# Performance work log

Hardware: AMD Instinct MI355X
Metric: run time of the kernel (lower is better)

Reference implementation:

```python
import jax, jax.numpy as jnp
import numpy as np
from jax.ops import segment_sum

N = 100000   # total nodes
M = 50000    # propagated subset size (len(index))
E = 600000   # edges over the subset graph
D = 128      # embedding_size
EPS = 1e-8
N_LAYERS = 3  # self.LayerNums


def setup_inputs() -> dict:
    key = jax.random.key(0)
    ks = jax.random.split(key, 12)
    features = jax.random.normal(ks[0], (N, D), dtype=jnp.float32)
    index = jnp.arange(M, dtype=jnp.int64)  # subset of nodes that get propagated
    edge_row = jax.random.randint(ks[1], (E,), 0, M, dtype=jnp.int64)
    edge_col = jax.random.randint(ks[2], (E,), 0, M, dtype=jnp.int64)
    edge_val = jax.random.uniform(ks[3], (E,), dtype=jnp.float32)
    # MLP prediction weights: D -> D//2 -> D//4 -> D//6 -> 1 (last no bias)
    def xavier(k, fan_in, fan_out):
        lim = jnp.sqrt(6.0 / (fan_in + fan_out)).astype(jnp.float32)
        return jax.random.uniform(k, (fan_in, fan_out), jnp.float32, -lim, lim)
    W1 = xavier(ks[4], D, D // 2); b1 = jnp.zeros((D // 2,), jnp.float32)
    W2 = xavier(ks[5], D // 2, D // 4); b2 = jnp.zeros((D // 4,), jnp.float32)
    W3 = xavier(ks[6], D // 4, D // 6); b3 = jnp.zeros((D // 6,), jnp.float32)
    W4 = xavier(ks[7], D // 6, 1)
    return {"features": features, "index": index, "edge_row": edge_row,
            "edge_col": edge_col, "edge_val": edge_val,
            "W1": W1, "b1": b1, "W2": W2, "b2": b2, "W3": W3, "b3": b3, "W4": W4}


def _gcn_layer(features, index, row, col, val):
    # symmetric normalization: d = rowsum(A)+eps; A' = d^-1/2 A d^-1/2
    deg = segment_sum(val, row, num_segments=M)
    d_inv_sqrt = jax.lax.rsqrt(deg + EPS)
    nval = val * d_inv_sqrt[row] * d_inv_sqrt[col]
    sub = features[index]                      # [M, D] subset_features
    msg = sub[col] * nval[:, None]             # [E, D]
    out = segment_sum(msg, row, num_segments=M)  # spmm -> [M, D]
    # new_features[index] = out; untouched rows keep original features
    return features.at[index].set(out)


def reference(features, index, edge_row, edge_col, edge_val,
              W1, b1, W2, b2, W3, b3, W4):
    x = features
    for _ in range(N_LAYERS):
        x = _gcn_layer(x, index, edge_row, edge_col, edge_val)
    # MLP prediction head (eval mode: dropout off), LeakyReLU slope 0.01
    h = jax.nn.leaky_relu(x @ W1 + b1, 0.01)
    h = jax.nn.leaky_relu(h @ W2 + b2, 0.01)
    h = jax.nn.leaky_relu(h @ W3 + b3, 0.01)
    return jax.nn.sigmoid(h @ W4)              # [N, 1]
```

## Files before the change

kernel.cpp:

```cpp
#include <hip/hip_runtime.h>
#include <math.h>

#define NN 100000
#define MM 50000
#define EE 600000
#define DD 128
#define NB 196
#define NNP 100096
#define EE4 750000

typedef short bf16x8 __attribute__((ext_vector_type(8)));
typedef float f32x4 __attribute__((ext_vector_type(4)));

__device__ __forceinline__ float bl(unsigned u) { return __uint_as_float(u << 16); }
__device__ __forceinline__ float bh(unsigned u) { return __uint_as_float(u & 0xFFFF0000u); }
__device__ __forceinline__ unsigned rne(float f) {
    unsigned u = __float_as_uint(f);
    return (u + 0x7FFFu + ((u >> 16) & 1u)) >> 16;
}
__device__ __forceinline__ unsigned pk2(float a, float b) { return rne(a) | (rne(b) << 16); }

__device__ __forceinline__ void fmab8(float v, uint4 u, float* a) {
    a[0] = fmaf(v, bl(u.x), a[0]); a[1] = fmaf(v, bh(u.x), a[1]);
    a[2] = fmaf(v, bl(u.y), a[2]); a[3] = fmaf(v, bh(u.y), a[3]);
    a[4] = fmaf(v, bl(u.z), a[4]); a[5] = fmaf(v, bh(u.z), a[5]);
    a[6] = fmaf(v, bl(u.w), a[6]); a[7] = fmaf(v, bh(u.w), a[7]);
}

__device__ __forceinline__ void fma21(float h, const float* wrow, float* a) {
    #pragma unroll
    for (int j = 0; j < 21; ++j) a[j] = fmaf(h, wrow[j], a[j]);
}

__global__ void deg_count_kernel(const int* __restrict__ row, const float* __restrict__ val,
                                 unsigned long long* __restrict__ dcpack,
                                 int* __restrict__ slot, int* __restrict__ invidx) {
    int e = blockIdx.x * 256 + threadIdx.x;
    if (e < NN) invidx[e] = -1;
    if (e < EE) {
        int r = row[e];
        unsigned long long add = (1ULL << 44) | (unsigned long long)(val[e] * 4294967296.0f);
        unsigned long long old = atomicAdd(&dcpack[r], add);
        slot[e] = (int)(old >> 44);
    }
}

__global__ void fused_setup_kernel(const unsigned long long* __restrict__ dcpack,
                                   float* __restrict__ dis,
                                   const int* __restrict__ index, int* __restrict__ invidx,
                                   int* __restrict__ cnt, int* __restrict__ blockhist) {
    __shared__ int lh[256];
    int tid = threadIdx.x;
    int i = blockIdx.x * 256 + tid;
    lh[tid] = 0;
    __syncthreads();
    if (i < MM) {
        unsigned long long pkv = dcpack[i];
        int v = (int)(pkv >> 44);
        float dsum = (float)(pkv & ((1ULL << 44) - 1)) * (1.0f / 4294967296.0f);
        dis[i] = rsqrtf(dsum + 1e-8f);
        invidx[index[i]] = i;
        cnt[i] = v;
        atomicAdd(&lh[min(v, 255)], 1);
    }
    __syncthreads();
    blockhist[tid * NB + blockIdx.x] = lh[tid];
}

__global__ void scan_bins_kernel(const int* __restrict__ blockhist,
                                 int* __restrict__ blockoff, int* __restrict__ total) {
    int d = blockIdx.x;
    int lane = threadIdx.x;
    int carry = 0;
    for (int base = 0; base < NB; base += 64) {
        int b = base + lane;
        int v = (b < NB) ? blockhist[d * NB + b] : 0;
        int x = v;
        #pragma unroll
        for (int off = 1; off < 64; off <<= 1) {
            int t = __shfl_up(x, off, 64);
            if (lane >= off) x += t;
        }
        if (b < NB) blockoff[d * NB + b] = carry + x - v;
        carry += __shfl(x, 63);
    }
    if (lane == 0) total[d] = carry;
}

__global__ void sort_rows_kernel(const int* __restrict__ cnt, const int* __restrict__ blockoff,
                                 const int* __restrict__ total, const int* __restrict__ index,
                                 int4* __restrict__ meta, int* __restrict__ row_s4) {
    __shared__ int lh[256], sbin[256], spad[256], ws[8];
    int tid = threadIdx.x, lane = tid & 63, w = tid >> 6;
    lh[tid] = 0;
    int t = total[tid];
    int v1 = t, v2 = t * ((tid + 3) & ~3);
    int x1 = v1, x2 = v2;
    #pragma unroll
    for (int off = 1; off < 64; off <<= 1) {
        int t1 = __shfl_up(x1, off, 64);
        int t2 = __shfl_up(x2, off, 64);
        if (lane >= off) { x1 += t1; x2 += t2; }
    }
    if (lane == 63) { ws[w] = x1; ws[4 + w] = x2; }
    __syncthreads();
    int a1 = 0, a2 = 0;
    for (int q = 0; q < w; ++q) { a1 += ws[q]; a2 += ws[4 + q]; }
    sbin[tid] = a1 + x1 - v1;
    spad[tid] = a2 + x2 - v2;
    __syncthreads();
    int i = blockIdx.x * 256 + tid;
    if (i < MM) {
        int d = cnt[i], c = min(d, 255);
        int lrank = atomicAdd(&lh[c], 1);
        int k = blockoff[c * NB + blockIdx.x] + lrank;
        int spos = sbin[c] + k;
        int s4 = spad[c] + k * ((d + 3) & ~3);
        meta[MM - 1 - spos] = make_int4(s4, d, i, index[i]);
        row_s4[i] = s4;
    }
}

__global__ void scatter_kernel(const int* __restrict__ row, const int* __restrict__ col,
                               const float* __restrict__ val, const float* __restrict__ dis,
                               const int* __restrict__ row_s4, const int* __restrict__ slot,
                               int* __restrict__ col_s, float* __restrict__ val_s) {
    int e = blockIdx.x * 256 + threadIdx.x;
    if (e < EE) {
        int r = row[e], c = col[e];
        int pos = row_s4[r] + slot[e];
        col_s[pos] = c;
        val_s[pos] = val[e] * dis[r] * dis[c];
    }
}

__global__ void cvt_kernel(const float* __restrict__ feat, const int* __restrict__ index,
                           const int* __restrict__ invidx,
                           unsigned* __restrict__ X0b, unsigned* __restrict__ Xfull,
                           const float* __restrict__ W1, const float* __restrict__ W2,
                           unsigned* __restrict__ W1b, unsigned* __restrict__ W2b) {
    int i = blockIdx.x * 256 + threadIdx.x;
    int n = i >> 6, u = i & 63;
    if (n < NN && invidx[n] < 0) {
        float2 f = ((const float2*)feat)[(size_t)n * 64 + u];
        Xfull[(size_t)n * 64 + u] = pk2(f.x, f.y);
    }
    if (i < MM * 64) {
        int idx = index[n];
        float2 f = ((const float2*)feat)[(size_t)idx * 64 + u];
        X0b[i] = pk2(f.x, f.y);
    }
    if (i < 4096) {
        int j = i >> 6, kp = i & 63;
        W1b[i] = pk2(W1[(2 * kp) * 64 + j], W1[(2 * kp + 1) * 64 + j]);
    } else if (i < 5120) {
        int t = i - 4096;
        int j = t >> 5, kp = t & 31;
        W2b[t] = pk2(W2[(2 * kp) * 32 + j], W2[(2 * kp + 1) * 32 + j]);
    }
}

__global__ __launch_bounds__(256) void spmm_kernel(
    const int4* __restrict__ meta, const int* __restrict__ cols,
    const float* __restrict__ vals, const unsigned short* __restrict__ X,
    unsigned short* __restrict__ Y, int use_remap) {
    int lane = threadIdx.x & 63;
    int wid = threadIdx.x >> 6;
    int g = lane >> 4, sub = lane & 15;
    int ri = blockIdx.x * 16 + wid * 4 + g;
    bool valid = (ri < MM);
    int rc = valid ? ri : (MM - 1);
    int4 mt = meta[rc];
    int s = mt.x, d = mt.y;
    const uint4* __restrict__ X4 = (const uint4*)X;
    float a[8] = {0.f, 0.f, 0.f, 0.f, 0.f, 0.f, 0.f, 0.f};
    int e4 = s + d;
    for (int base = s; base < e4; base += 4) {
        int4 c4 = *(const int4*)(cols + base);
        float4 v4 = *(const float4*)(vals + base);
        uint4 u0 = X4[c4.x * 16 + sub];
        uint4 u1 = X4[c4.y * 16 + sub];
        uint4 u2 = X4[c4.z * 16 + sub];
        uint4 u3 = X4[c4.w * 16 + sub];
        fmab8(v4.x, u0, a);
        fmab8(v4.y, u1, a);
        fmab8(v4.z, u2, a);
        fmab8(v4.w, u3, a);
    }
    if (valid) {
        int dst = use_remap ? mt.w : mt.z;
        uint4 o;
        o.x = pk2(a[0], a[1]); o.y = pk2(a[2], a[3]);
        o.z = pk2(a[4], a[5]); o.w = pk2(a[6], a[7]);
        ((uint4*)Y)[dst * 16 + sub] = o;
    }
}

__global__ __launch_bounds__(256) void mlp_kernel(
    const unsigned* __restrict__ Xfull,
    const unsigned* __restrict__ W1b, const float* __restrict__ b1,
    const unsigned* __restrict__ W2b, const float* __restrict__ b2,
    const float* __restrict__ W3, const float* __restrict__ b3,
    const float* __restrict__ W4, float* __restrict__ out) {
    __shared__ float hls[4 * 1088];
    int tid = threadIdx.x;
    int lane = tid & 63, w = tid >> 6;
    int p = lane & 15, q = lane >> 4;
    float* hw = hls + w * 1088;
    int nb = blockIdx.x * 64;
    int node = nb + w * 16 + p;

    bf16x8 af[4];
    #pragma unroll
    for (int kc = 0; kc < 4; ++kc) {
        uint4 u = *(const uint4*)(Xfull + (size_t)node * 64 + kc * 16 + q * 4);
        af[kc] = *(const bf16x8*)&u;
    }
    f32x4 acc[4];
    #pragma unroll
    for (int jt = 0; jt < 4; ++jt) {
        float bv = b1[jt * 16 + p];
        acc[jt][0] = bv; acc[jt][1] = bv; acc[jt][2] = bv; acc[jt][3] = bv;
    }
    #pragma unroll
    for (int jt = 0; jt < 4; ++jt) {
        #pragma unroll
        for (int kc = 0; kc < 4; ++kc) {
            uint4 u = *(const uint4*)(W1b + (jt * 16 + p) * 64 + kc * 16 + q * 4);
            bf16x8 bf = *(const bf16x8*)&u;
            acc[jt] = __builtin_amdgcn_mfma_f32_16x16x32_bf16(af[kc], bf, acc[jt], 0, 0, 0);
        }
    }
    #pragma unroll
    for (int jt = 0; jt < 4; ++jt) {
        #pragma unroll
        for (int r = 0; r < 4; ++r) {
            float v = acc[jt][r];
            v = v > 0.f ? v : 0.01f * v;
            hw[(q * 4 + r) * 68 + jt * 16 + p] = v;
        }
    }
    bf16x8 a2f[2];
    #pragma unroll
    for (int kc = 0; kc < 2; ++kc) {
        const float* hp = hw + p * 68 + kc * 32 + q * 8;
        f32x4 v0 = *(const f32x4*)hp;
        f32x4 v1 = *(const f32x4*)(hp + 4);
        uint4 uu = make_uint4(pk2(v0[0], v0[1]), pk2(v0[2], v0[3]),
                              pk2(v1[0], v1[1]), pk2(v1[2], v1[3]));
        a2f[kc] = *(const bf16x8*)&uu;
    }
    f32x4 acc2[2];
    #pragma unroll
    for (int jt = 0; jt < 2; ++jt) {
        float bv = b2[jt * 16 + p];
        acc2[jt][0] = bv; acc2[jt][1] = bv; acc2[jt][2] = bv; acc2[jt][3] = bv;
        #pragma unroll
        for (int kc = 0; kc < 2; ++kc) {
            uint4 u = *(const uint4*)(W2b + (jt * 16 + p) * 32 + kc * 16 + q * 4);
            bf16x8 bf = *(const bf16x8*)&u;
            acc2[jt] = __builtin_amdgcn_mfma_f32_16x16x32_bf16(a2f[kc], bf, acc2[jt], 0, 0, 0);
        }
    }
    #pragma unroll
    for (int jt = 0; jt < 2; ++jt) {
        #pragma unroll
        for (int r = 0; r < 4; ++r) {
            float v = acc2[jt][r];
            v = v > 0.f ? v : 0.01f * v;
            hw[(q * 4 + r) * 36 + jt * 16 + p] = v;
        }
    }
    float a3[21];
    #pragma unroll
    for (int j = 0; j < 21; ++j) a3[j] = b3[j];
    #pragma unroll 4
    for (int k = 0; k < 32; ++k) {
        float hk = hw[p * 36 + k];
        fma21(hk, W3 + k * 21, a3);
    }
    float s = 0.f;
    #pragma unroll
    for (int j = 0; j < 21; ++j) {
        float vj = a3[j] > 0.f ? a3[j] : 0.01f * a3[j];
        s = fmaf(vj, W4[j], s);
    }
    if (q == 0) {
        int n = nb + w * 16 + p;
        if (n < NN) out[n] = 1.f / (1.f + expf(-s));
    }
}

extern "C" void kernel_launch(void* const* d_in, const int* in_sizes, int n_in,
                              void* d_out, int out_size, void* d_ws, size_t ws_size,
                              hipStream_t stream) {
    const float* feat = (const float*)d_in[0];
    const int*   index = (const int*)d_in[1];
    const int*   erow = (const int*)d_in[2];
    const int*   ecol = (const int*)d_in[3];
    const float* evalp = (const float*)d_in[4];
    const float* W1 = (const float*)d_in[5];
    const float* b1 = (const float*)d_in[6];
    const float* W2 = (const float*)d_in[7];
    const float* b2 = (const float*)d_in[8];
    const float* W3 = (const float*)d_in[9];
    const float* b3 = (const float*)d_in[10];
    const float* W4 = (const float*)d_in[11];
    float* out = (float*)d_out;

    char* ws = (char*)d_ws;
    size_t off = 0;
    auto alloc = [&](size_t bytes) -> void* {
        void* p = ws + off;
        off += (bytes + 255) & ~(size_t)255;
        return p;
    };
    unsigned long long* dcpack = (unsigned long long*)alloc((size_t)MM * 8);
    int*   col_s   = (int*)  alloc((size_t)EE4 * 4);
    float* val_s   = (float*)alloc((size_t)EE4 * 4);
    size_t zero_span = (size_t)((char*)val_s - (char*)dcpack) + (size_t)EE4 * 4;

    float* dis     = (float*)alloc((size_t)MM * 4);
    int*   cnt     = (int*)  alloc((size_t)MM * 4);
    int*   slot    = (int*)  alloc((size_t)EE * 4);
    int*   invidx  = (int*)  alloc((size_t)NN * 4);
    int*   row_s4  = (int*)  alloc((size_t)MM * 4);
    int*   blockhist = (int*)alloc((size_t)256 * NB * 4);
    int*   blockoff  = (int*)alloc((size_t)256 * NB * 4);
    int*   total     = (int*)alloc((size_t)256 * 4);
    int4*  meta      = (int4*)alloc((size_t)MM * 16);
    unsigned* W1b  = (unsigned*)alloc(4096 * 4);
    unsigned* W2b  = (unsigned*)alloc(1024 * 4);
    unsigned*       X0b   = (unsigned*)      alloc((size_t)MM * DD * 2);
    unsigned short* Xa    = (unsigned short*)alloc((size_t)MM * DD * 2);
    unsigned short* Xb    = (unsigned short*)alloc((size_t)MM * DD * 2);
    unsigned*       Xfull = (unsigned*)      alloc((size_t)NNP * DD * 2);

    hipMemsetAsync(dcpack, 0, zero_span, stream);

    deg_count_kernel<<<(EE + 255) / 256, 256, 0, stream>>>(erow, evalp, dcpack, slot, invidx);
    fused_setup_kernel<<<NB, 256, 0, stream>>>(dcpack, dis, index, invidx, cnt, blockhist);
    scan_bins_kernel<<<256, 64, 0, stream>>>(blockhist, blockoff, total);
    sort_rows_kernel<<<NB, 256, 0, stream>>>(cnt, blockoff, total, index, meta, row_s4);
    scatter_kernel<<<(EE + 255) / 256, 256, 0, stream>>>(erow, ecol, evalp, dis,
                                                         row_s4, slot, col_s, val_s);
    cvt_kernel<<<(NN * 64 + 255) / 256, 256, 0, stream>>>(feat, index, invidx, X0b, Xfull,
                                                          W1, W2, W1b, W2b);

    spmm_kernel<<<(MM + 15) / 16, 256, 0, stream>>>(meta, col_s, val_s,
                                                    (const unsigned short*)X0b, Xa, 0);
    spmm_kernel<<<(MM + 15) / 16, 256, 0, stream>>>(meta, col_s, val_s, Xa, Xb, 0);
    spmm_kernel<<<(MM + 15) / 16, 256, 0, stream>>>(meta, col_s, val_s, Xb,
                                                    (unsigned short*)Xfull, 1);

    mlp_kernel<<<(NNP + 63) / 64, 256, 0, stream>>>(Xfull, W1b, b1, W2b, b2,
                                                    W3, b3, W4, out);
}
```

Before: 270.8 us.

## Fuse front-end kernels and merge setup stages into a cooperative grid-sync kernel

Merges the degree-count atomics, the feature and weight conversion into bf16, and writing the full feature buffer into one front kernel. The per-row setup, histogram scan, row sort and edge scatter become a single cooperative kernel separated by grid.sync, replacing five launches. The memset now covers only the packed degree array, and padding slots are zeroed explicitly. Xfull is now written for every row, including subset rows that the last spmm overwrites, so extra bandwidth is traded for dropping the invidx lookup. The cooperative launch needs all 196 blocks resident at once.

```diff
diff --git a/kernel.cpp b/kernel.cpp
--- a/kernel.cpp
+++ b/kernel.cpp
@@ -1,5 +1,8 @@
 #include <hip/hip_runtime.h>
+#include <hip/hip_cooperative_groups.h>
 #include <math.h>
+
+namespace cg = cooperative_groups;
 
 #define NN 100000
 #define MM 50000
@@ -32,26 +35,54 @@
     for (int j = 0; j < 21; ++j) a[j] = fmaf(h, wrow[j], a[j]);
 }
 
-__global__ void deg_count_kernel(const int* __restrict__ row, const float* __restrict__ val,
-                                 unsigned long long* __restrict__ dcpack,
-                                 int* __restrict__ slot, int* __restrict__ invidx) {
-    int e = blockIdx.x * 256 + threadIdx.x;
-    if (e < NN) invidx[e] = -1;
-    if (e < EE) {
-        int r = row[e];
-        unsigned long long add = (1ULL << 44) | (unsigned long long)(val[e] * 4294967296.0f);
+__global__ __launch_bounds__(256) void fused_front_kernel(
+    const int* __restrict__ row, const float* __restrict__ val,
+    unsigned long long* __restrict__ dcpack, int* __restrict__ slot,
+    const float* __restrict__ feat, const int* __restrict__ index,
+    unsigned* __restrict__ X0b, unsigned* __restrict__ Xfull,
+    const float* __restrict__ W1, const float* __restrict__ W2,
+    unsigned* __restrict__ W1b, unsigned* __restrict__ W2b) {
+    int i = blockIdx.x * 256 + threadIdx.x;
+    int n = i >> 6, u = i & 63;
+    {
+        float2 f = ((const float2*)feat)[(size_t)n * 64 + u];
+        Xfull[(size_t)n * 64 + u] = pk2(f.x, f.y);
+    }
+    if (i < MM * 64) {
+        int idx = index[n];
+        float2 f = ((const float2*)feat)[(size_t)idx * 64 + u];
+        X0b[i] = pk2(f.x, f.y);
+    }
+    if (i < 4096) {
+        int j = i >> 6, kp = i & 63;
+        W1b[i] = pk2(W1[(2 * kp) * 64 + j], W1[(2 * kp + 1) * 64 + j]);
+    } else if (i < 5120) {
+        int t = i - 4096;
+        int j = t >> 5, kp = t & 31;
+        W2b[t] = pk2(W2[(2 * kp) * 32 + j], W2[(2 * kp + 1) * 32 + j]);
+    }
+    if (i < EE) {
+        int r = row[i];
+        unsigned long long add = (1ULL << 44) | (unsigned long long)(val[i] * 4294967296.0f);
         unsigned long long old = atomicAdd(&dcpack[r], add);
-        slot[e] = (int)(old >> 44);
-    }
-}
-
-__global__ void fused_setup_kernel(const unsigned long long* __restrict__ dcpack,
-                                   float* __restrict__ dis,
-                                   const int* __restrict__ index, int* __restrict__ invidx,
-                                   int* __restrict__ cnt, int* __restrict__ blockhist) {
-    __shared__ int lh[256];
-    int tid = threadIdx.x;
-    int i = blockIdx.x * 256 + tid;
+        slot[i] = (int)(old >> 44);
+    }
+}
+
+__global__ __launch_bounds__(256) void prep_kernel(
+    const unsigned long long* __restrict__ dcpack, float* __restrict__ dis,
+    const int* __restrict__ index, int* __restrict__ cnt,
+    int* __restrict__ blockhist, int* __restrict__ blockoff, int* __restrict__ total,
+    int4* __restrict__ meta, int* __restrict__ row_s4,
+    const int* __restrict__ erow, const int* __restrict__ ecol,
+    const float* __restrict__ evalp, const int* __restrict__ slot,
+    int* __restrict__ col_s, float* __restrict__ val_s) {
+    cg::grid_group grid = cg::this_grid();
+    __shared__ int lh[256], sbin[256], spad[256], ws[8];
+    int tid = threadIdx.x, lane = tid & 63, w = tid >> 6;
+    int b = blockIdx.x;
+    int i = b * 256 + tid;
+
     lh[tid] = 0;
     __syncthreads();
     if (i < MM) {
@@ -59,39 +90,32 @@
         int v = (int)(pkv >> 44);
         float dsum = (float)(pkv & ((1ULL << 44) - 1)) * (1.0f / 4294967296.0f);
         dis[i] = rsqrtf(dsum + 1e-8f);
-        invidx[index[i]] = i;
         cnt[i] = v;
         atomicAdd(&lh[min(v, 255)], 1);
     }
     __syncthreads();
-    blockhist[tid * NB + blockIdx.x] = lh[tid];
-}
-
-__global__ void scan_bins_kernel(const int* __restrict__ blockhist,
-                                 int* __restrict__ blockoff, int* __restrict__ total) {
-    int d = blockIdx.x;
-    int lane = threadIdx.x;
-    int carry = 0;
-    for (int base = 0; base < NB; base += 64) {
-        int b = base + lane;
-        int v = (b < NB) ? blockhist[d * NB + b] : 0;
-        int x = v;
-        #pragma unroll
-        for (int off = 1; off < 64; off <<= 1) {
-            int t = __shfl_up(x, off, 64);
-            if (lane >= off) x += t;
-        }
-        if (b < NB) blockoff[d * NB + b] = carry + x - v;
-        carry += __shfl(x, 63);
-    }
-    if (lane == 0) total[d] = carry;
-}
-
-__global__ void sort_rows_kernel(const int* __restrict__ cnt, const int* __restrict__ blockoff,
-                                 const int* __restrict__ total, const int* __restrict__ index,
-                                 int4* __restrict__ meta, int* __restrict__ row_s4) {
-    __shared__ int lh[256], sbin[256], spad[256], ws[8];
-    int tid = threadIdx.x, lane = tid & 63, w = tid >> 6;
+    blockhist[tid * NB + b] = lh[tid];
+    grid.sync();
+
+    if (b < 64) {
+        int d = b * 4 + w;
+        int carry = 0;
+        for (int base = 0; base < NB; base += 64) {
+            int bb = base + lane;
+            int v = (bb < NB) ? blockhist[d * NB + bb] : 0;
+            int x = v;
+            #pragma unroll
+            for (int off = 1; off < 64; off <<= 1) {
+                int t = __shfl_up(x, off, 64);
+                if (lane >= off) x += t;
+            }
+            if (bb < NB) blockoff[d * NB + bb] = carry + x - v;
+            carry += __shfl(x, 63);
+        }
+        if (lane == 0) total[d] = carry;
+    }
+    grid.sync();
+
     lh[tid] = 0;
     int t = total[tid];
     int v1 = t, v2 = t * ((tid + 3) & ~3);
@@ -109,54 +133,24 @@
     sbin[tid] = a1 + x1 - v1;
     spad[tid] = a2 + x2 - v2;
     __syncthreads();
-    int i = blockIdx.x * 256 + tid;
     if (i < MM) {
         int d = cnt[i], c = min(d, 255);
         int lrank = atomicAdd(&lh[c], 1);
-        int k = blockoff[c * NB + blockIdx.x] + lrank;
+        int k = blockoff[c * NB + b] + lrank;
         int spos = sbin[c] + k;
         int s4 = spad[c] + k * ((d + 3) & ~3);
         meta[MM - 1 - spos] = make_int4(s4, d, i, index[i]);
         row_s4[i] = s4;
-    }
-}
-
-__global__ void scatter_kernel(const int* __restrict__ row, const int* __restrict__ col,
-                               const float* __restrict__ val, const float* __restrict__ dis,
-                               const int* __restrict__ row_s4, const int* __restrict__ slot,
-                               int* __restrict__ col_s, float* __restrict__ val_s) {
-    int e = blockIdx.x * 256 + threadIdx.x;
-    if (e < EE) {
-        int r = row[e], c = col[e];
+        int p4 = (d + 3) & ~3;
+        for (int pp = d; pp < p4; ++pp) { col_s[s4 + pp] = 0; val_s[s4 + pp] = 0.f; }
+    }
+    grid.sync();
+
+    for (int e = i; e < EE; e += NB * 256) {
+        int r = erow[e], c = ecol[e];
         int pos = row_s4[r] + slot[e];
         col_s[pos] = c;
-        val_s[pos] = val[e] * dis[r] * dis[c];
-    }
-}
-
-__global__ void cvt_kernel(const float* __restrict__ feat, const int* __restrict__ index,
-                           const int* __restrict__ invidx,
-                           unsigned* __restrict__ X0b, unsigned* __restrict__ Xfull,
-                           const float* __restrict__ W1, const float* __restrict__ W2,
-                           unsigned* __restrict__ W1b, unsigned* __restrict__ W2b) {
-    int i = blockIdx.x * 256 + threadIdx.x;
-    int n = i >> 6, u = i & 63;
-    if (n < NN && invidx[n] < 0) {
-        float2 f = ((const float2*)feat)[(size_t)n * 64 + u];
-        Xfull[(size_t)n * 64 + u] = pk2(f.x, f.y);
-    }
-    if (i < MM * 64) {
-        int idx = index[n];
-        float2 f = ((const float2*)feat)[(size_t)idx * 64 + u];
-        X0b[i] = pk2(f.x, f.y);
-    }
-    if (i < 4096) {
-        int j = i >> 6, kp = i & 63;
-        W1b[i] = pk2(W1[(2 * kp) * 64 + j], W1[(2 * kp + 1) * 64 + j]);
-    } else if (i < 5120) {
-        int t = i - 4096;
-        int j = t >> 5, kp = t & 31;
-        W2b[t] = pk2(W2[(2 * kp) * 32 + j], W2[(2 * kp + 1) * 32 + j]);
+        val_s[pos] = evalp[e] * dis[r] * dis[c];
     }
 }
 
@@ -318,12 +312,9 @@
     unsigned long long* dcpack = (unsigned long long*)alloc((size_t)MM * 8);
     int*   col_s   = (int*)  alloc((size_t)EE4 * 4);
     float* val_s   = (float*)alloc((size_t)EE4 * 4);
-    size_t zero_span = (size_t)((char*)val_s - (char*)dcpack) + (size_t)EE4 * 4;
-
     float* dis     = (float*)alloc((size_t)MM * 4);
     int*   cnt     = (int*)  alloc((size_t)MM * 4);
     int*   slot    = (int*)  alloc((size_t)EE * 4);
-    int*   invidx  = (int*)  alloc((size_t)NN * 4);
     int*   row_s4  = (int*)  alloc((size_t)MM * 4);
     int*   blockhist = (int*)alloc((size_t)256 * NB * 4);
     int*   blockoff  = (int*)alloc((size_t)256 * NB * 4);
@@ -336,16 +327,17 @@
     unsigned short* Xb    = (unsigned short*)alloc((size_t)MM * DD * 2);
     unsigned*       Xfull = (unsigned*)      alloc((size_t)NNP * DD * 2);
 
-    hipMemsetAsync(dcpack, 0, zero_span, stream);
-
-    deg_count_kernel<<<(EE + 255) / 256, 256, 0, stream>>>(erow, evalp, dcpack, slot, invidx);
-    fused_setup_kernel<<<NB, 256, 0, stream>>>(dcpack, dis, index, invidx, cnt, blockhist);
-    scan_bins_kernel<<<256, 64, 0, stream>>>(blockhist, blockoff, total);
-    sort_rows_kernel<<<NB, 256, 0, stream>>>(cnt, blockoff, total, index, meta, row_s4);
-    scatter_kernel<<<(EE + 255) / 256, 256, 0, stream>>>(erow, ecol, evalp, dis,
-                                                         row_s4, slot, col_s, val_s);
-    cvt_kernel<<<(NN * 64 + 255) / 256, 256, 0, stream>>>(feat, index, invidx, X0b, Xfull,
-                                                          W1, W2, W1b, W2b);
+    hipMemsetAsync(dcpack, 0, (size_t)MM * 8, stream);
+
+    fused_front_kernel<<<(NN * 64) / 256, 256, 0, stream>>>(
+        erow, evalp, dcpack, slot, feat, index, X0b, Xfull, W1, W2, W1b, W2b);
+
+    {
+        void* args[] = { &dcpack, &dis, &index, &cnt, &blockhist, &blockoff, &total,
+                         &meta, &row_s4, &erow, &ecol, &evalp, &slot, &col_s, &val_s };
+        hipLaunchCooperativeKernel((const void*)prep_kernel, dim3(NB), dim3(256),
+                                   args, 0, stream);
+    }
 
     spmm_kernel<<<(MM + 15) / 16, 256, 0, stream>>>(meta, col_s, val_s,
                                                     (const unsigned short*)X0b, Xa, 0);
```

Result: slower. 373.0 us (+37.7%).

## Split SpMM features into XCD-pinned column quarters and interleave col/val pairs

Applied to the files above, without the earlier changes.

Feature matrices for the SpMM layers are stored as four column-quarter planes. Each block is mapped by blockIdx to a quarter so that blocks on the same pair of XCDs share one quarter, keeping its gather working set small enough to stay in their L2. Column indices and values are packed into one int2 array, and pad entries are zeroed in the sort kernel rather than by a large memset. The degree-count and conversion kernels are fused into one front kernel that writes all of Xfull unconditionally, removing the invidx pass. The cost is four times as many SpMM blocks, each re-reading the edge lists, and narrower 4-byte gathers.

```diff
diff --git a/kernel.cpp b/kernel.cpp
--- a/kernel.cpp
+++ b/kernel.cpp
@@ -20,35 +20,48 @@
 }
 __device__ __forceinline__ unsigned pk2(float a, float b) { return rne(a) | (rne(b) << 16); }
 
-__device__ __forceinline__ void fmab8(float v, uint4 u, float* a) {
-    a[0] = fmaf(v, bl(u.x), a[0]); a[1] = fmaf(v, bh(u.x), a[1]);
-    a[2] = fmaf(v, bl(u.y), a[2]); a[3] = fmaf(v, bh(u.y), a[3]);
-    a[4] = fmaf(v, bl(u.z), a[4]); a[5] = fmaf(v, bh(u.z), a[5]);
-    a[6] = fmaf(v, bl(u.w), a[6]); a[7] = fmaf(v, bh(u.w), a[7]);
-}
-
 __device__ __forceinline__ void fma21(float h, const float* wrow, float* a) {
     #pragma unroll
     for (int j = 0; j < 21; ++j) a[j] = fmaf(h, wrow[j], a[j]);
 }
 
-__global__ void deg_count_kernel(const int* __restrict__ row, const float* __restrict__ val,
-                                 unsigned long long* __restrict__ dcpack,
-                                 int* __restrict__ slot, int* __restrict__ invidx) {
-    int e = blockIdx.x * 256 + threadIdx.x;
-    if (e < NN) invidx[e] = -1;
-    if (e < EE) {
-        int r = row[e];
-        unsigned long long add = (1ULL << 44) | (unsigned long long)(val[e] * 4294967296.0f);
+__global__ __launch_bounds__(256) void front_kernel(
+    const int* __restrict__ row, const float* __restrict__ val,
+    unsigned long long* __restrict__ dcpack, int* __restrict__ slot,
+    const float* __restrict__ feat, const int* __restrict__ index,
+    unsigned* __restrict__ X0b, unsigned* __restrict__ Xfull,
+    const float* __restrict__ W1, const float* __restrict__ W2,
+    unsigned* __restrict__ W1b, unsigned* __restrict__ W2b) {
+    int i = blockIdx.x * 256 + threadIdx.x;
+    int n = i >> 6, u = i & 63;
+    {
+        float2 f = ((const float2*)feat)[(size_t)n * 64 + u];
+        Xfull[(size_t)n * 64 + u] = pk2(f.x, f.y);
+    }
+    if (i < MM * 64) {
+        int idx = index[n];
+        float2 f = ((const float2*)feat)[(size_t)idx * 64 + u];
+        X0b[((size_t)(u >> 4) * MM + n) * 16 + (u & 15)] = pk2(f.x, f.y);
+    }
+    if (i < 4096) {
+        int j = i >> 6, kp = i & 63;
+        W1b[i] = pk2(W1[(2 * kp) * 64 + j], W1[(2 * kp + 1) * 64 + j]);
+    } else if (i < 5120) {
+        int t = i - 4096;
+        int j = t >> 5, kp = t & 31;
+        W2b[t] = pk2(W2[(2 * kp) * 32 + j], W2[(2 * kp + 1) * 32 + j]);
+    }
+    if (i < EE) {
+        int r = row[i];
+        unsigned long long add = (1ULL << 44) | (unsigned long long)(val[i] * 4294967296.0f);
         unsigned long long old = atomicAdd(&dcpack[r], add);
-        slot[e] = (int)(old >> 44);
-    }
-}
-
-__global__ void fused_setup_kernel(const unsigned long long* __restrict__ dcpack,
-                                   float* __restrict__ dis,
-                                   const int* __restrict__ index, int* __restrict__ invidx,
-                                   int* __restrict__ cnt, int* __restrict__ blockhist) {
+        slot[i] = (int)(old >> 44);
+    }
+}
+
+__global__ void setup_kernel(const unsigned long long* __restrict__ dcpack,
+                             float* __restrict__ dis, int* __restrict__ cnt,
+                             int* __restrict__ blockhist) {
     __shared__ int lh[256];
     int tid = threadIdx.x;
     int i = blockIdx.x * 256 + tid;
@@ -59,7 +72,6 @@
         int v = (int)(pkv >> 44);
         float dsum = (float)(pkv & ((1ULL << 44) - 1)) * (1.0f / 4294967296.0f);
         dis[i] = rsqrtf(dsum + 1e-8f);
-        invidx[index[i]] = i;
         cnt[i] = v;
         atomicAdd(&lh[min(v, 255)], 1);
     }
@@ -67,8 +79,8 @@
     blockhist[tid * NB + blockIdx.x] = lh[tid];
 }
 
-__global__ void scan_bins_kernel(const int* __restrict__ blockhist,
-                                 int* __restrict__ blockoff, int* __restrict__ total) {
+__global__ void scan_kernel(const int* __restrict__ blockhist,
+                            int* __restrict__ blockoff, int* __restrict__ total) {
     int d = blockIdx.x;
     int lane = threadIdx.x;
     int carry = 0;
@@ -87,9 +99,10 @@
     if (lane == 0) total[d] = carry;
 }
 
-__global__ void sort_rows_kernel(const int* __restrict__ cnt, const int* __restrict__ blockoff,
-                                 const int* __restrict__ total, const int* __restrict__ index,
-                                 int4* __restrict__ meta, int* __restrict__ row_s4) {
+__global__ void sort_kernel(const int* __restrict__ cnt, const int* __restrict__ blockoff,
+                            const int* __restrict__ total, const int* __restrict__ index,
+                            int4* __restrict__ meta, int* __restrict__ row_s4,
+                            int2* __restrict__ cv_s) {
     __shared__ int lh[256], sbin[256], spad[256], ws[8];
     int tid = threadIdx.x, lane = tid & 63, w = tid >> 6;
     lh[tid] = 0;
@@ -118,81 +131,61 @@
         int s4 = spad[c] + k * ((d + 3) & ~3);
         meta[MM - 1 - spos] = make_int4(s4, d, i, index[i]);
         row_s4[i] = s4;
+        int p4 = (d + 3) & ~3;
+        for (int pp = d; pp < p4; ++pp) cv_s[s4 + pp] = make_int2(0, 0);
     }
 }
 
 __global__ void scatter_kernel(const int* __restrict__ row, const int* __restrict__ col,
                                const float* __restrict__ val, const float* __restrict__ dis,
                                const int* __restrict__ row_s4, const int* __restrict__ slot,
-                               int* __restrict__ col_s, float* __restrict__ val_s) {
+                               int2* __restrict__ cv_s) {
     int e = blockIdx.x * 256 + threadIdx.x;
     if (e < EE) {
         int r = row[e], c = col[e];
         int pos = row_s4[r] + slot[e];
-        col_s[pos] = c;
-        val_s[pos] = val[e] * dis[r] * dis[c];
-    }
-}
-
-__global__ void cvt_kernel(const float* __restrict__ feat, const int* __restrict__ index,
-                           const int* __restrict__ invidx,
-                           unsigned* __restrict__ X0b, unsigned* __restrict__ Xfull,
-                           const float* __restrict__ W1, const float* __restrict__ W2,
-                           unsigned* __restrict__ W1b, unsigned* __restrict__ W2b) {
-    int i = blockIdx.x * 256 + threadIdx.x;
-    int n = i >> 6, u = i & 63;
-    if (n < NN && invidx[n] < 0) {
-        float2 f = ((const float2*)feat)[(size_t)n * 64 + u];
-        Xfull[(size_t)n * 64 + u] = pk2(f.x, f.y);
-    }
-    if (i < MM * 64) {
-        int idx = index[n];
-        float2 f = ((const float2*)feat)[(size_t)idx * 64 + u];
-        X0b[i] = pk2(f.x, f.y);
-    }
-    if (i < 4096) {
-        int j = i >> 6, kp = i & 63;
-        W1b[i] = pk2(W1[(2 * kp) * 64 + j], W1[(2 * kp + 1) * 64 + j]);
-    } else if (i < 5120) {
-        int t = i - 4096;
-        int j = t >> 5, kp = t & 31;
-        W2b[t] = pk2(W2[(2 * kp) * 32 + j], W2[(2 * kp + 1) * 32 + j]);
-    }
-}
-
-__global__ __launch_bounds__(256) void spmm_kernel(
-    const int4* __restrict__ meta, const int* __restrict__ cols,
-    const float* __restrict__ vals, const unsigned short* __restrict__ X,
-    unsigned short* __restrict__ Y, int use_remap) {
-    int lane = threadIdx.x & 63;
-    int wid = threadIdx.x >> 6;
+        cv_s[pos] = make_int2(c, __float_as_int(val[e] * dis[r] * dis[c]));
+    }
+}
+
+template <int TAG>
+__global__ __launch_bounds__(256) void spmmq_kernel(
+    const int4* __restrict__ meta, const int2* __restrict__ cv,
+    const unsigned* __restrict__ X, unsigned* __restrict__ Y, int last) {
+    int b = blockIdx.x;
+    int xcd = b & 7;
+    int q = xcd >> 1;
+    int vb = ((b >> 3) << 1) + (xcd & 1);
+    if (vb >= (MM + 15) / 16) return;
+    int lane = threadIdx.x & 63, wid = threadIdx.x >> 6;
     int g = lane >> 4, sub = lane & 15;
-    int ri = blockIdx.x * 16 + wid * 4 + g;
+    int ri = vb * 16 + wid * 4 + g;
     bool valid = (ri < MM);
     int rc = valid ? ri : (MM - 1);
     int4 mt = meta[rc];
     int s = mt.x, d = mt.y;
-    const uint4* __restrict__ X4 = (const uint4*)X;
-    float a[8] = {0.f, 0.f, 0.f, 0.f, 0.f, 0.f, 0.f, 0.f};
+    const uint4* __restrict__ CV = (const uint4*)cv;
+    const unsigned* __restrict__ Xq = X + (size_t)q * (MM * 16);
+    float a0 = 0.f, a1 = 0.f;
     int e4 = s + d;
     for (int base = s; base < e4; base += 4) {
-        int4 c4 = *(const int4*)(cols + base);
-        float4 v4 = *(const float4*)(vals + base);
-        uint4 u0 = X4[c4.x * 16 + sub];
-        uint4 u1 = X4[c4.y * 16 + sub];
-        uint4 u2 = X4[c4.z * 16 + sub];
-        uint4 u3 = X4[c4.w * 16 + sub];
-        fmab8(v4.x, u0, a);
-        fmab8(v4.y, u1, a);
-        fmab8(v4.z, u2, a);
-        fmab8(v4.w, u3, a);
+        uint4 p0 = CV[(base >> 1)];
+        uint4 p1 = CV[(base >> 1) + 1];
+        unsigned u0 = Xq[(int)p0.x * 16 + sub];
+        unsigned u1 = Xq[(int)p0.z * 16 + sub];
+        unsigned u2 = Xq[(int)p1.x * 16 + sub];
+        unsigned u3 = Xq[(int)p1.z * 16 + sub];
+        float v0 = __uint_as_float(p0.y), v1 = __uint_as_float(p0.w);
+        float v2 = __uint_as_float(p1.y), v3 = __uint_as_float(p1.w);
+        a0 = fmaf(v0, bl(u0), a0); a1 = fmaf(v0, bh(u0), a1);
+        a0 = fmaf(v1, bl(u1), a0); a1 = fmaf(v1, bh(u1), a1);
+        a0 = fmaf(v2, bl(u2), a0); a1 = fmaf(v2, bh(u2), a1);
+        a0 = fmaf(v3, bl(u3), a0); a1 = fmaf(v3, bh(u3), a1);
     }
     if (valid) {
-        int dst = use_remap ? mt.w : mt.z;
-        uint4 o;
-        o.x = pk2(a[0], a[1]); o.y = pk2(a[2], a[3]);
-        o.z = pk2(a[4], a[5]); o.w = pk2(a[6], a[7]);
-        ((uint4*)Y)[dst * 16 + sub] = o;
+        unsigned o = pk2(a0, a1);
+        if (last) Y[(size_t)mt.w * 64 + q * 16 + sub] = o;
+        else      Y[(size_t)q * (MM * 16) + (size_t)mt.z * 16 + sub] = o;
     }
 }
 
@@ -316,14 +309,10 @@
         return p;
     };
     unsigned long long* dcpack = (unsigned long long*)alloc((size_t)MM * 8);
-    int*   col_s   = (int*)  alloc((size_t)EE4 * 4);
-    float* val_s   = (float*)alloc((size_t)EE4 * 4);
-    size_t zero_span = (size_t)((char*)val_s - (char*)dcpack) + (size_t)EE4 * 4;
-
+    int2*  cv_s    = (int2*) alloc((size_t)EE4 * 8);
     float* dis     = (float*)alloc((size_t)MM * 4);
     int*   cnt     = (int*)  alloc((size_t)MM * 4);
     int*   slot    = (int*)  alloc((size_t)EE * 4);
-    int*   invidx  = (int*)  alloc((size_t)NN * 4);
     int*   row_s4  = (int*)  alloc((size_t)MM * 4);
     int*   blockhist = (int*)alloc((size_t)256 * NB * 4);
     int*   blockoff  = (int*)alloc((size_t)256 * NB * 4);
@@ -332,26 +321,24 @@
     unsigned* W1b  = (unsigned*)alloc(4096 * 4);
     unsigned* W2b  = (unsigned*)alloc(1024 * 4);
     unsigned*       X0b   = (unsigned*)      alloc((size_t)MM * DD * 2);
-    unsigned short* Xa    = (unsigned short*)alloc((size_t)MM * DD * 2);
-    unsigned short* Xb    = (unsigned short*)alloc((size_t)MM * DD * 2);
+    unsigned*       Xa    = (unsigned*)      alloc((size_t)MM * DD * 2);
+    unsigned*       Xb    = (unsigned*)      alloc((size_t)MM * DD * 2);
     unsigned*       Xfull = (unsigned*)      alloc((size_t)NNP * DD * 2);
 
-    hipMemsetAsync(dcpack, 0, zero_span, stream);
-
-    deg_count_kernel<<<(EE + 255) / 256, 256, 0, stream>>>(erow, evalp, dcpack, slot, invidx);
-    fused_setup_kernel<<<NB, 256, 0, stream>>>(dcpack, dis, index, invidx, cnt, blockhist);
-    scan_bins_kernel<<<256, 64, 0, stream>>>(blockhist, blockoff, total);
-    sort_rows_kernel<<<NB, 256, 0, stream>>>(cnt, blockoff, total, index, meta, row_s4);
+    hipMemsetAsync(dcpack, 0, (size_t)MM * 8, stream);
+
+    front_kernel<<<(NN * 64) / 256, 256, 0, stream>>>(
+        erow, evalp, dcpack, slot, feat, index, X0b, Xfull, W1, W2, W1b, W2b);
+    setup_kernel<<<NB, 256, 0, stream>>>(dcpack, dis, cnt, blockhist);
+    scan_kernel<<<256, 64, 0, stream>>>(blockhist, blockoff, total);
+    sort_kernel<<<NB, 256, 0, stream>>>(cnt, blockoff, total, index, meta, row_s4, cv_s);
     scatter_kernel<<<(EE + 255) / 256, 256, 0, stream>>>(erow, ecol, evalp, dis,
-                                                         row_s4, slot, col_s, val_s);
-    cvt_kernel<<<(NN * 64 + 255) / 256, 256, 0, stream>>>(feat, index, invidx, X0b, Xfull,
-                                                          W1, W2, W1b, W2b);
-
-    spmm_kernel<<<(MM + 15) / 16, 256, 0, stream>>>(meta, col_s, val_s,
-                                                    (const unsigned short*)X0b, Xa, 0);
-    spmm_kernel<<<(MM + 15) / 16, 256, 0, stream>>>(meta, col_s, val_s, Xa, Xb, 0);
-    spmm_kernel<<<(MM + 15) / 16, 256, 0, stream>>>(meta, col_s, val_s, Xb,
-                                                    (unsigned short*)Xfull, 1);
+                                                         row_s4, slot, cv_s);
+
+    const int NGRID = (((MM + 15) / 16 + 1) / 2) * 8 + 8;
+    spmmq_kernel<0><<<NGRID, 256, 0, stream>>>(meta, cv_s, X0b, Xa, 0);
+    spmmq_kernel<1><<<NGRID, 256, 0, stream>>>(meta, cv_s, Xa, Xb, 0);
+    spmmq_kernel<2><<<NGRID, 256, 0, stream>>>(meta, cv_s, Xb, Xfull, 1);
 
     mlp_kernel<<<(NNP + 63) / 64, 256, 0, stream>>>(Xfull, W1b, b1, W2b, b2,
                                                     W3, b3, W4, out);
```

After: 273.6 us. About the same (+1.0%).
